# Kernel optimization log

Measured on AMD Instinct MI355X. Metric: run time of the kernel, lower is better.

## Reference

```python
import jax, jax.numpy as jnp
import numpy as np

N = 50000
E = 800000
IN_DIM, HID, OUT = 128, 256, 40
BN_EPS = 1e-5


def setup_inputs() -> dict:
    key = jax.random.key(0)
    ks = jax.random.split(key, 10)
    x = jax.random.normal(ks[0], (N, IN_DIM), dtype=jnp.float32)
    edge_index = jax.random.randint(ks[1], (2, E), 0, N, dtype=jnp.int64)
    W1 = jax.random.normal(ks[2], (IN_DIM, HID), dtype=jnp.float32) * 0.05
    b1 = jnp.zeros((HID,), dtype=jnp.float32)
    W2 = jax.random.normal(ks[3], (HID, HID), dtype=jnp.float32) * 0.05
    b2 = jnp.zeros((HID,), dtype=jnp.float32)
    W3 = jax.random.normal(ks[4], (HID, OUT), dtype=jnp.float32) * 0.05
    b3 = jnp.zeros((OUT,), dtype=jnp.float32)
    # BatchNorm params (shared across the two pre-final layers in the source)
    gamma = jnp.ones((HID,), dtype=jnp.float32)
    beta = jnp.zeros((HID,), dtype=jnp.float32)
    return {"x": x, "edge_index": edge_index, "W1": W1, "b1": b1,
            "W2": W2, "b2": b2, "W3": W3, "b3": b3,
            "gamma": gamma, "beta": beta}


def _gcn_norm(edge_index):
    # add self-loops, compute symmetric normalization D^-1/2 (A+I) D^-1/2
    self_loops = jnp.arange(N, dtype=edge_index.dtype)
    row = jnp.concatenate([edge_index[0], self_loops])
    col = jnp.concatenate([edge_index[1], self_loops])
    deg = jax.ops.segment_sum(jnp.ones_like(row, dtype=jnp.float32), col, num_segments=N)
    dinv = jnp.where(deg > 0, jax.lax.rsqrt(deg), 0.0)
    norm = dinv[row] * dinv[col]  # [E+N]
    return row, col, norm


def _gcn_conv(h, W, b, row, col, norm):
    h = h @ W                              # transform first (smaller msg dim)
    msg = norm[:, None] * h[col]           # [E+N, F] gather
    agg = jax.ops.segment_sum(msg, row, num_segments=N)  # scatter-add
    return agg + b


def _batchnorm(h, gamma, beta):
    mu = jnp.mean(h, axis=0)
    var = jnp.mean((h - mu) ** 2, axis=0)
    return (h - mu) * jax.lax.rsqrt(var + BN_EPS) * gamma + beta


def reference(x, edge_index, W1, b1, W2, b2, W3, b3, gamma, beta):
    row, col, norm = _gcn_norm(edge_index)
    out = _gcn_conv(x, W1, b1, row, col, norm)
    out = jax.nn.relu(_batchnorm(out, gamma, beta))
    out = _gcn_conv(out, W2, b2, row, col, norm)
    out = jax.nn.relu(_batchnorm(out, gamma, beta))  # BN shared in source
    out = _gcn_conv(out, W3, b3, row, col, norm)
    return jax.nn.log_softmax(out, axis=-1)
```

## Files before the change

### kernel.cpp

```cpp
#include <hip/hip_runtime.h>
#include <math.h>

#define NN 50000
#define NE 800000
#define IN_DIM 128
#define HID 256
#define OUT_DIM 40
#define BN_EPS 1e-5f

#define HG 128
#define HW 25000
#define HPASS 12800

#define NBK 196
#define PB 256
#define EPB (NE / PB)

typedef __attribute__((ext_vector_type(8))) short short8;
typedef __attribute__((ext_vector_type(4))) float f32x4;
typedef __attribute__((ext_vector_type(2))) float f32x2;

__device__ __forceinline__ ushort f2bf(float f) {
    union { float f; unsigned u; } v; v.f = f;
    unsigned r = v.u + 0x7fffu + ((v.u >> 16) & 1u);
    return (ushort)(r >> 16);
}
__device__ __forceinline__ unsigned pack2bf(float a, float b) {
    return (unsigned)f2bf(a) | ((unsigned)f2bf(b) << 16);
}
__device__ __forceinline__ float bflo(unsigned u) {
    union { unsigned a; float f; } v; v.a = u << 16; return v.f;
}
__device__ __forceinline__ float bfhi(unsigned u) {
    union { unsigned a; float f; } v; v.a = u & 0xffff0000u; return v.f;
}
__device__ __forceinline__ f32x2 fp8_dec_lo(int v) {
    return __builtin_amdgcn_cvt_pk_f32_fp8(v, false);
}
__device__ __forceinline__ f32x2 fp8_dec_hi(int v) {
    return __builtin_amdgcn_cvt_pk_f32_fp8(v, true);
}
__device__ __forceinline__ int fp8_enc_lo(float a, float b, int old) {
    return __builtin_amdgcn_cvt_pk_fp8_f32(a, b, old, false);
}
__device__ __forceinline__ int fp8_enc_hi(float a, float b, int old) {
    return __builtin_amdgcn_cvt_pk_fp8_f32(a, b, old, true);
}

__global__ __launch_bounds__(512) void k_p1(const int* __restrict__ erow,
                                            const int* __restrict__ ecol,
                                            unsigned* __restrict__ Pcol,
                                            unsigned* __restrict__ cnt) {
    __shared__ unsigned lds[HPASS];
    int t = threadIdx.x;
    int b = blockIdx.x;
    if (b < HG) {
        unsigned* partial = Pcol + (size_t)b * HW;
        int e0 = b * (NE / HG), e1 = e0 + (NE / HG);
#pragma unroll
        for (int pass = 0; pass < 2; pass++) {
            int wbase = pass ? HPASS : 0;
            int wend = pass ? HW : HPASS;
            int nw = wend - wbase;
            for (int w = t; w < HPASS; w += 512) lds[w] = 0u;
            __syncthreads();
            int vlo = wbase * 2, vhi = wend * 2;
            for (int e = e0 + t; e < e1; e += 512) {
                int v = ecol[e];
                if (v >= vlo && v < vhi)
                    atomicAdd(&lds[(v >> 1) - wbase], (v & 1) ? 0x10000u : 1u);
            }
            __syncthreads();
            for (int w = t; w < nw; w += 512) partial[wbase + w] = lds[w];
            __syncthreads();
        }
    } else {
        int bb = b - HG;
        for (int i = t; i < NBK; i += 512) lds[i] = 0u;
        __syncthreads();
        int e0 = bb * EPB;
        for (int i = t; i < EPB; i += 512) atomicAdd(&lds[((unsigned)erow[e0 + i]) >> 8], 1u);
        __syncthreads();
        for (int i = t; i < NBK; i += 512) cnt[bb * NBK + i] = lds[i];
    }
}

__global__ __launch_bounds__(256) void k_p2(const unsigned* __restrict__ Pcol,
                                            float* __restrict__ dinv,
                                            const unsigned* __restrict__ cnt,
                                            unsigned* __restrict__ off,
                                            unsigned* __restrict__ bstart,
                                            float* __restrict__ bnacc) {
    int t = threadIdx.x;
    if (blockIdx.x < 98) {
        int w = blockIdx.x * 256 + t;
        if (w >= HW) return;
        unsigned sc = 0;
        for (int b = 0; b < HG; b++) sc += Pcol[(size_t)b * HW + w];
        dinv[2 * w] = rsqrtf((float)((sc & 0xffffu) + 1u));
        dinv[2 * w + 1] = rsqrtf((float)((sc >> 16) + 1u));
    } else if (blockIdx.x == 98) {
        __shared__ unsigned s[256];
        unsigned tot = 0;
        if (t < NBK) for (int b = 0; b < PB; b++) tot += cnt[b * NBK + t];
        s[t] = tot;
        __syncthreads();
        for (int o = 1; o < 256; o <<= 1) {
            unsigned x = (t >= o) ? s[t - o] : 0u;
            __syncthreads();
            s[t] += x;
            __syncthreads();
        }
        unsigned base = s[t] - tot;
        if (t < NBK) bstart[t] = base;
        if (t == NBK - 1) bstart[NBK] = base + tot;
        if (t < NBK) {
            unsigned run = base;
            for (int b = 0; b < PB; b++) { off[b * NBK + t] = run; run += cnt[b * NBK + t]; }
        }
    } else {
        bnacc[(blockIdx.x - 99) * 256 + t] = 0.f;
    }
}

__global__ __launch_bounds__(256) void k_p3(const int* __restrict__ erow,
                                            const int* __restrict__ ecol,
                                            const unsigned* __restrict__ off,
                                            int2* __restrict__ ebuf,
                                            const float* __restrict__ x,
                                            const float* __restrict__ dinv,
                                            uchar* __restrict__ xs8,
                                            const float* __restrict__ W1,
                                            const float* __restrict__ W2,
                                            const float* __restrict__ W3,
                                            ushort* __restrict__ Wt1,
                                            ushort* __restrict__ Wt2,
                                            ushort* __restrict__ Wt3) {
    int t = threadIdx.x, b = blockIdx.x;
    if (b < PB) {
        __shared__ unsigned c[NBK];
        for (int i = t; i < NBK; i += 256) c[i] = off[b * NBK + i];
        __syncthreads();
        int e0 = b * EPB;
        for (int i = t; i < EPB; i += 256) {
            int r = erow[e0 + i], cc = ecol[e0 + i];
            unsigned p = atomicAdd(&c[((unsigned)r) >> 8], 1u);
            ebuf[p] = make_int2(r, cc);
        }
    } else if (b < PB + 6250) {
        int i = (b - PB) * 256 + t;
        int row = i >> 5;
        float d = dinv[row];
        float4 v = ((const float4*)x)[i];
        int p = fp8_enc_lo(v.x * d, v.y * d, 0);
        p = fp8_enc_hi(v.z * d, v.w * d, p);
        ((int*)xs8)[i] = p;
    } else {
        int i = (b - PB - 6250) * 256 + t;
        if (i < 128 * 256) { int k = i / 256, n = i % 256; Wt1[n * 128 + k] = f2bf(W1[i]); }
        if (i < 256 * 256) { int k = i / 256, n = i % 256; Wt2[n * 256 + k] = f2bf(W2[i]); }
        if (i < 48 * 256)  { int n = i / 256, k = i % 256;
                             Wt3[i] = (n < OUT_DIM) ? f2bf(W3[k * OUT_DIM + n]) : (ushort)0; }
    }
}

__global__ __launch_bounds__(256) void k_part4(const int2* __restrict__ ebuf,
                                               const unsigned* __restrict__ bstart,
                                               unsigned* __restrict__ rowptr,
                                               int* __restrict__ colidx) {
    __shared__ unsigned rc[256], cur[256], s[256];
    int t = threadIdx.x, b = blockIdx.x;
    unsigned ebase = bstart[b], ecnt = bstart[b + 1] - ebase;
    rc[t] = 0u;
    __syncthreads();
    for (unsigned i = t; i < ecnt; i += 256) atomicAdd(&rc[ebuf[ebase + i].x & 255], 1u);
    __syncthreads();
    unsigned v = rc[t];
    s[t] = v;
    __syncthreads();
    for (int o = 1; o < 256; o <<= 1) {
        unsigned x = (t >= o) ? s[t - o] : 0u;
        __syncthreads();
        s[t] += x;
        __syncthreads();
    }
    unsigned excl = s[t] - v;
    int row = (b << 8) + t;
    if (row < NN) rowptr[row] = ebase + excl;
    cur[t] = ebase + excl;
    if (b == 0 && t == 0) rowptr[NN] = NE;
    __syncthreads();
    for (unsigned i = t; i < ecnt; i += 256) {
        int2 e = ebuf[ebase + i];
        unsigned p = atomicAdd(&cur[e.x & 255], 1u);
        colidx[p] = e.y;
    }
}

__global__ __launch_bounds__(64) void k_agg_x(const uchar* __restrict__ xs8,
                                              const unsigned* __restrict__ rowptr,
                                              const int* __restrict__ colidx,
                                              const float* __restrict__ dinv,
                                              ushort* __restrict__ Xa) {
    int r = blockIdx.x;
    int t = threadIdx.x;
    int lane = t & 31, half = t >> 5;
    const unsigned* Xv = (const unsigned*)xs8;
    float a0 = 0.f, a1 = 0.f, a2 = 0.f, a3 = 0.f;
    if (half == 0) {
        unsigned y = Xv[(size_t)r * 32 + lane];
        f32x2 l = fp8_dec_lo((int)y), h = fp8_dec_hi((int)y);
        a0 = l[0]; a1 = l[1]; a2 = h[0]; a3 = h[1];
    }
    unsigned e0 = rowptr[r], e1 = rowptr[r + 1];
    unsigned e = e0 + half;
    for (; e + 6 < e1; e += 8) {
        int c0 = colidx[e], c1 = colidx[e + 2], c2 = colidx[e + 4], c3 = colidx[e + 6];
        unsigned v0 = Xv[(size_t)c0 * 32 + lane];
        unsigned v1 = Xv[(size_t)c1 * 32 + lane];
        unsigned v2 = Xv[(size_t)c2 * 32 + lane];
        unsigned v3 = Xv[(size_t)c3 * 32 + lane];
        f32x2 l0 = fp8_dec_lo((int)v0), h0 = fp8_dec_hi((int)v0);
        f32x2 l1 = fp8_dec_lo((int)v1), h1 = fp8_dec_hi((int)v1);
        f32x2 l2 = fp8_dec_lo((int)v2), h2 = fp8_dec_hi((int)v2);
        f32x2 l3 = fp8_dec_lo((int)v3), h3 = fp8_dec_hi((int)v3);
        a0 += l0[0] + l1[0] + l2[0] + l3[0];
        a1 += l0[1] + l1[1] + l2[1] + l3[1];
        a2 += h0[0] + h1[0] + h2[0] + h3[0];
        a3 += h0[1] + h1[1] + h2[1] + h3[1];
    }
    for (; e < e1; e += 2) {
        unsigned v = Xv[(size_t)colidx[e] * 32 + lane];
        f32x2 l = fp8_dec_lo((int)v), h = fp8_dec_hi((int)v);
        a0 += l[0]; a1 += l[1]; a2 += h[0]; a3 += h[1];
    }
    a0 += __shfl_xor(a0, 32, 64);
    a1 += __shfl_xor(a1, 32, 64);
    a2 += __shfl_xor(a2, 32, 64);
    a3 += __shfl_xor(a3, 32, 64);
    if (half == 0) {
        float dr = dinv[r];
        uint2 o;
        o.x = pack2bf(dr * a0, dr * a1);
        o.y = pack2bf(dr * a2, dr * a3);
        ((uint2*)Xa)[(size_t)r * 32 + lane] = o;
    }
}

template <int K>
__global__ __launch_bounds__(256) void k_gemm1(const ushort* __restrict__ A,
                                               const ushort* __restrict__ Bt,
                                               ushort* __restrict__ H16,
                                               float* __restrict__ bnacc) {
    constexpr int BK = 32;
    constexpr int LD = 40;
    __shared__ ushort sA[64 * LD];
    __shared__ ushort sB[128 * LD];
    int t = threadIdx.x;
    int wave = t >> 6, lane = t & 63;
    int quad = lane >> 4, m15 = lane & 15;
    long r0 = (long)blockIdx.x * 64;
    int n0 = blockIdx.y * 128;

    f32x4 acc[8];
#pragma unroll
    for (int i = 0; i < 8; i++) { acc[i][0] = 0.f; acc[i][1] = 0.f; acc[i][2] = 0.f; acc[i][3] = 0.f; }

    for (int k0 = 0; k0 < K; k0 += BK) {
        {
            int row = t >> 2, seg = (t & 3) * 8;
            long gr = r0 + row;
            uint4 v = make_uint4(0, 0, 0, 0);
            if (gr < NN) v = *(const uint4*)(A + gr * K + k0 + seg);
            *(uint4*)(sA + row * LD + seg) = v;
        }
        {
            int n = t >> 1, seg = (t & 1) * 16;
            const uint4* src = (const uint4*)(Bt + (long)(n0 + n) * K + k0 + seg);
            uint4 b0 = src[0], b1 = src[1];
            *(uint4*)(sB + n * LD + seg) = b0;
            *(uint4*)(sB + n * LD + seg + 8) = b1;
        }
        __syncthreads();
        short8 a = *(const short8*)(sA + (wave * 16 + m15) * LD + quad * 8);
#pragma unroll
        for (int ct = 0; ct < 8; ct++) {
            short8 b = *(const short8*)(sB + (ct * 16 + m15) * LD + quad * 8);
            acc[ct] = __builtin_amdgcn_mfma_f32_16x16x32_bf16(a, b, acc[ct], 0, 0, 0);
        }
        __syncthreads();
    }
    long rowbase = r0 + wave * 16 + quad * 4;
#pragma unroll
    for (int ct = 0; ct < 8; ct++) {
        int col = n0 + ct * 16 + m15;
#pragma unroll
        for (int rg = 0; rg < 4; rg++) {
            long gr = rowbase + rg;
            if (gr < NN) H16[gr * 256 + col] = f2bf(acc[ct][rg]);
        }
    }
    float* ldsS = (float*)(void*)sA;
    float* ldsQ = (float*)(void*)sB;
#pragma unroll
    for (int ct = 0; ct < 8; ct++) {
        float s = acc[ct][0] + acc[ct][1] + acc[ct][2] + acc[ct][3];
        float q = acc[ct][0] * acc[ct][0] + acc[ct][1] * acc[ct][1]
                + acc[ct][2] * acc[ct][2] + acc[ct][3] * acc[ct][3];
        s += __shfl_xor(s, 16, 64); q += __shfl_xor(q, 16, 64);
        s += __shfl_xor(s, 32, 64); q += __shfl_xor(q, 32, 64);
        if (quad == 0) {
            ldsS[wave * 128 + ct * 16 + m15] = s;
            ldsQ[wave * 128 + ct * 16 + m15] = q;
        }
    }
    __syncthreads();
    {
        int c = t & 127;
        int slice = blockIdx.x & 7;
        float v = (t < 128)
            ? ldsS[c] + ldsS[128 + c] + ldsS[256 + c] + ldsS[384 + c]
            : ldsQ[c] + ldsQ[128 + c] + ldsQ[256 + c] + ldsQ[384 + c];
        atomicAdd(&bnacc[slice * 512 + ((t < 128) ? 0 : 256) + n0 + c], v);
    }
}

__device__ __forceinline__ void bn_prolog(const float* __restrict__ bnacc,
                                          const float* __restrict__ gamma,
                                          const float* __restrict__ beta,
                                          float* __restrict__ bnsc,
                                          float* __restrict__ bnsh, int t) {
    float s = 0.f, q = 0.f;
#pragma unroll
    for (int sl = 0; sl < 8; sl++) {
        s += bnacc[sl * 512 + t];
        q += bnacc[sl * 512 + 256 + t];
    }
    float mu = s * (1.f / NN);
    float var = q * (1.f / NN) - mu * mu;
    float g = gamma[t] * rsqrtf(var + BN_EPS);
    bnsc[t] = g;
    bnsh[t] = beta[t] - mu * g;
}

__device__ __forceinline__ void bn_stage8(const ushort* __restrict__ Hrow, bool valid,
                                          const float* __restrict__ bnsc,
                                          const float* __restrict__ bnsh, int col0,
                                          ushort* __restrict__ dst) {
    uint4 hv = make_uint4(0, 0, 0, 0);
    if (valid) hv = *(const uint4*)(Hrow + col0);
    float f[8] = { bflo(hv.x), bfhi(hv.x), bflo(hv.y), bfhi(hv.y),
                   bflo(hv.z), bfhi(hv.z), bflo(hv.w), bfhi(hv.w) };
#pragma unroll
    for (int j = 0; j < 8; j++)
        dst[j] = f2bf(fmaxf(f[j] * bnsc[col0 + j] + bnsh[col0 + j], 0.f));
}

__global__ __launch_bounds__(256) void k_gemm2(const ushort* __restrict__ H16,
                                               const float* __restrict__ bnacc,
                                               const float* __restrict__ gamma,
                                               const float* __restrict__ beta,
                                               const ushort* __restrict__ Bt,
                                               const float* __restrict__ dinv,
                                               uchar* __restrict__ Y8) {
    constexpr int K = 256, BK = 32, LD = 40;
    __shared__ ushort sA[64 * LD];
    __shared__ ushort sB[128 * LD];
    __shared__ float bnsc[256], bnsh[256];
    int t = threadIdx.x;
    int wave = t >> 6, lane = t & 63;
    int quad = lane >> 4, m15 = lane & 15;
    long r0 = (long)blockIdx.x * 64;
    int n0 = blockIdx.y * 128;

    bn_prolog(bnacc, gamma, beta, bnsc, bnsh, t);
    __syncthreads();

    f32x4 acc[8];
#pragma unroll
    for (int i = 0; i < 8; i++) { acc[i][0] = 0.f; acc[i][1] = 0.f; acc[i][2] = 0.f; acc[i][3] = 0.f; }

    for (int k0 = 0; k0 < K; k0 += BK) {
        {
            int row = t >> 2, seg = (t & 3) * 8;
            long gr = r0 + row;
            bn_stage8(H16 + gr * 256, gr < NN, bnsc, bnsh, k0 + seg, sA + row * LD + seg);
        }
        {
            int n = t >> 1, seg = (t & 1) * 16;
            const uint4* src = (const uint4*)(Bt + (long)(n0 + n) * K + k0 + seg);
            uint4 b0 = src[0], b1 = src[1];
            *(uint4*)(sB + n * LD + seg) = b0;
            *(uint4*)(sB + n * LD + seg + 8) = b1;
        }
        __syncthreads();
        short8 a = *(const short8*)(sA + (wave * 16 + m15) * LD + quad * 8);
#pragma unroll
        for (int ct = 0; ct < 8; ct++) {
            short8 b = *(const short8*)(sB + (ct * 16 + m15) * LD + quad * 8);
            acc[ct] = __builtin_amdgcn_mfma_f32_16x16x32_bf16(a, b, acc[ct], 0, 0, 0);
        }
        __syncthreads();
    }
    long rowbase = r0 + wave * 16 + quad * 4;
    float dv[4];
#pragma unroll
    for (int rg = 0; rg < 4; rg++) dv[rg] = (rowbase + rg < NN) ? dinv[rowbase + rg] : 0.f;
#pragma unroll
    for (int ct = 0; ct < 8; ct++) {
        int col = n0 + ct * 16 + m15;
#pragma unroll
        for (int rg = 0; rg < 4; rg++) {
            long gr = rowbase + rg;
            if (gr < NN) {
                int p = fp8_enc_lo(dv[rg] * acc[ct][rg], 0.f, 0);
                Y8[gr * 256 + col] = (uchar)(p & 0xff);
            }
        }
    }
}

__global__ __launch_bounds__(256) void k_gemm3(const ushort* __restrict__ H16,
                                               const float* __restrict__ bnacc,
                                               const float* __restrict__ gamma,
                                               const float* __restrict__ beta,
                                               const ushort* __restrict__ Wt3,
                                               const float* __restrict__ dinv,
                                               ushort* __restrict__ Y) {
    constexpr int LD = 264;
    __shared__ ushort sA[64 * LD];
    __shared__ ushort sB[48 * LD];
    __shared__ float bnsc[256], bnsh[256];
    int t = threadIdx.x;
    int wave = t >> 6, lane = t & 63;
    int quad = lane >> 4, m15 = lane & 15;
    long r0 = (long)blockIdx.x * 64;

    bn_prolog(bnacc, gamma, beta, bnsc, bnsh, t);
    __syncthreads();

    for (int idx = t; idx < 48 * 16; idx += 256) {
        int n = idx >> 4, s = (idx & 15) * 16;
        const uint4* src = (const uint4*)(Wt3 + n * 256 + s);
        *(uint4*)(sB + n * LD + s) = src[0];
        *(uint4*)(sB + n * LD + s + 8) = src[1];
    }
    {
        int row = t >> 2;
        long gr = r0 + row;
#pragma unroll
        for (int s8 = 0; s8 < 8; s8++) {
            int seg = s8 * 32 + (t & 3) * 8;
            bn_stage8(H16 + gr * 256, gr < NN, bnsc, bnsh, seg, sA + row * LD + seg);
        }
    }
    __syncthreads();

    f32x4 acc[3];
#pragma unroll
    for (int i = 0; i < 3; i++) { acc[i][0] = 0.f; acc[i][1] = 0.f; acc[i][2] = 0.f; acc[i][3] = 0.f; }
#pragma unroll
    for (int k0 = 0; k0 < 256; k0 += 32) {
        short8 a = *(const short8*)(sA + (wave * 16 + m15) * LD + k0 + quad * 8);
#pragma unroll
        for (int ct = 0; ct < 3; ct++) {
            short8 b = *(const short8*)(sB + (ct * 16 + m15) * LD + k0 + quad * 8);
            acc[ct] = __builtin_amdgcn_mfma_f32_16x16x32_bf16(a, b, acc[ct], 0, 0, 0);
        }
    }
    long rowbase = r0 + wave * 16 + quad * 4;
#pragma unroll
    for (int ct = 0; ct < 3; ct++) {
        int col = ct * 16 + m15;
#pragma unroll
        for (int rg = 0; rg < 4; rg++) {
            long gr = rowbase + rg;
            if (gr < NN) Y[gr * 64 + col] = f2bf(dinv[gr] * acc[ct][rg]);
        }
    }
}

__global__ __launch_bounds__(64) void k_agg_hid(const uchar* __restrict__ Y8,
                                                const unsigned* __restrict__ rowptr,
                                                const int* __restrict__ colidx,
                                                const float* __restrict__ dinv,
                                                ushort* __restrict__ H16) {
    int r = blockIdx.x;
    int t = threadIdx.x;
    int lane = t & 31, half = t >> 5;
    const uint2* Yv = (const uint2*)Y8;
    float a0 = 0.f, a1 = 0.f, a2 = 0.f, a3 = 0.f, a4 = 0.f, a5 = 0.f, a6 = 0.f, a7 = 0.f;
    if (half == 0) {
        uint2 y = Yv[(size_t)r * 32 + lane];
        f32x2 p0 = fp8_dec_lo((int)y.x), p1 = fp8_dec_hi((int)y.x);
        f32x2 p2 = fp8_dec_lo((int)y.y), p3 = fp8_dec_hi((int)y.y);
        a0 = p0[0]; a1 = p0[1]; a2 = p1[0]; a3 = p1[1];
        a4 = p2[0]; a5 = p2[1]; a6 = p3[0]; a7 = p3[1];
    }
    unsigned e0 = rowptr[r], e1 = rowptr[r + 1];
    unsigned e = e0 + half;
    for (; e + 6 < e1; e += 8) {
        int c0 = colidx[e], c1 = colidx[e + 2], c2 = colidx[e + 4], c3 = colidx[e + 6];
        uint2 v0 = Yv[(size_t)c0 * 32 + lane];
        uint2 v1 = Yv[(size_t)c1 * 32 + lane];
        uint2 v2 = Yv[(size_t)c2 * 32 + lane];
        uint2 v3 = Yv[(size_t)c3 * 32 + lane];
        f32x2 l0x = fp8_dec_lo((int)v0.x), h0x = fp8_dec_hi((int)v0.x);
        f32x2 l0y = fp8_dec_lo((int)v0.y), h0y = fp8_dec_hi((int)v0.y);
        f32x2 l1x = fp8_dec_lo((int)v1.x), h1x = fp8_dec_hi((int)v1.x);
        f32x2 l1y = fp8_dec_lo((int)v1.y), h1y = fp8_dec_hi((int)v1.y);
        f32x2 l2x = fp8_dec_lo((int)v2.x), h2x = fp8_dec_hi((int)v2.x);
        f32x2 l2y = fp8_dec_lo((int)v2.y), h2y = fp8_dec_hi((int)v2.y);
        f32x2 l3x = fp8_dec_lo((int)v3.x), h3x = fp8_dec_hi((int)v3.x);
        f32x2 l3y = fp8_dec_lo((int)v3.y), h3y = fp8_dec_hi((int)v3.y);
        a0 += l0x[0] + l1x[0] + l2x[0] + l3x[0];
        a1 += l0x[1] + l1x[1] + l2x[1] + l3x[1];
        a2 += h0x[0] + h1x[0] + h2x[0] + h3x[0];
        a3 += h0x[1] + h1x[1] + h2x[1] + h3x[1];
        a4 += l0y[0] + l1y[0] + l2y[0] + l3y[0];
        a5 += l0y[1] + l1y[1] + l2y[1] + l3y[1];
        a6 += h0y[0] + h1y[0] + h2y[0] + h3y[0];
        a7 += h0y[1] + h1y[1] + h2y[1] + h3y[1];
    }
    for (; e < e1; e += 2) {
        uint2 v = Yv[(size_t)colidx[e] * 32 + lane];
        f32x2 lx = fp8_dec_lo((int)v.x), hx = fp8_dec_hi((int)v.x);
        f32x2 ly = fp8_dec_lo((int)v.y), hy = fp8_dec_hi((int)v.y);
        a0 += lx[0]; a1 += lx[1]; a2 += hx[0]; a3 += hx[1];
        a4 += ly[0]; a5 += ly[1]; a6 += hy[0]; a7 += hy[1];
    }
    a0 += __shfl_xor(a0, 32, 64); a1 += __shfl_xor(a1, 32, 64);
    a2 += __shfl_xor(a2, 32, 64); a3 += __shfl_xor(a3, 32, 64);
    a4 += __shfl_xor(a4, 32, 64); a5 += __shfl_xor(a5, 32, 64);
    a6 += __shfl_xor(a6, 32, 64); a7 += __shfl_xor(a7, 32, 64);
    if (half == 0) {
        float dr = dinv[r];
        uint4 o;
        o.x = pack2bf(dr * a0, dr * a1);
        o.y = pack2bf(dr * a2, dr * a3);
        o.z = pack2bf(dr * a4, dr * a5);
        o.w = pack2bf(dr * a6, dr * a7);
        ((uint4*)H16)[(size_t)r * 32 + lane] = o;
    }
}

__global__ __launch_bounds__(64) void k_agg_lsm(const ushort* __restrict__ Y,
                                                const unsigned* __restrict__ rowptr,
                                                const int* __restrict__ colidx,
                                                const float* __restrict__ dinv,
                                                const float* __restrict__ b3,
                                                float* __restrict__ out) {
    int r = blockIdx.x;
    int t = threadIdx.x;
    int lane = t & 31, half = t >> 5;
    const unsigned* Yv = (const unsigned*)Y;
    float a0 = 0.f, a1 = 0.f;
    if (half == 0) {
        unsigned y = Yv[(size_t)r * 32 + lane];
        a0 = bflo(y); a1 = bfhi(y);
    }
    unsigned e0 = rowptr[r], e1 = rowptr[r + 1];
    unsigned e = e0 + half;
    for (; e + 6 < e1; e += 8) {
        int c0 = colidx[e], c1 = colidx[e + 2], c2 = colidx[e + 4], c3 = colidx[e + 6];
        unsigned v0 = Yv[(size_t)c0 * 32 + lane];
        unsigned v1 = Yv[(size_t)c1 * 32 + lane];
        unsigned v2 = Yv[(size_t)c2 * 32 + lane];
        unsigned v3 = Yv[(size_t)c3 * 32 + lane];
        a0 += bflo(v0) + bflo(v1) + bflo(v2) + bflo(v3);
        a1 += bfhi(v0) + bfhi(v1) + bfhi(v2) + bfhi(v3);
    }
    for (; e < e1; e += 2) {
        unsigned v = Yv[(size_t)colidx[e] * 32 + lane];
        a0 += bflo(v); a1 += bfhi(v);
    }
    a0 += __shfl_xor(a0, 32, 64);
    a1 += __shfl_xor(a1, 32, 64);
    bool act = (half == 0) && (lane < OUT_DIM / 2);
    float o0 = -1e30f, o1 = -1e30f;
    if (act) {
        float dr = dinv[r];
        o0 = dr * a0 + b3[2 * lane];
        o1 = dr * a1 + b3[2 * lane + 1];
    }
    float m = fmaxf(o0, o1);
#pragma unroll
    for (int d = 1; d < 64; d <<= 1) m = fmaxf(m, __shfl_xor(m, d, 64));
    float ex = act ? (expf(o0 - m) + expf(o1 - m)) : 0.f;
#pragma unroll
    for (int d = 1; d < 64; d <<= 1) ex += __shfl_xor(ex, d, 64);
    float ls = logf(ex) + m;
    if (act) {
        out[(size_t)r * OUT_DIM + 2 * lane] = o0 - ls;
        out[(size_t)r * OUT_DIM + 2 * lane + 1] = o1 - ls;
    }
}

__global__ __launch_bounds__(256) void k_bn_stats2(const ushort* __restrict__ H16,
                                                   float* __restrict__ bnacc) {
    __shared__ float ls[512];
    int t = threadIdx.x;
    ls[t] = 0.f; ls[t + 256] = 0.f;
    __syncthreads();
    int colb = (t & 31) * 8;
    float s[8], q[8];
#pragma unroll
    for (int j = 0; j < 8; j++) { s[j] = 0.f; q[j] = 0.f; }
    for (int rb = blockIdx.x * 8 + (t >> 5); rb < NN; rb += gridDim.x * 8) {
        uint4 v = *(const uint4*)(H16 + (size_t)rb * 256 + colb);
        float f[8] = { bflo(v.x), bfhi(v.x), bflo(v.y), bfhi(v.y),
                       bflo(v.z), bfhi(v.z), bflo(v.w), bfhi(v.w) };
#pragma unroll
        for (int j = 0; j < 8; j++) { s[j] += f[j]; q[j] += f[j] * f[j]; }
    }
#pragma unroll
    for (int j = 0; j < 8; j++) {
        atomicAdd(&ls[colb + j], s[j]);
        atomicAdd(&ls[256 + colb + j], q[j]);
    }
    __syncthreads();
    int slice = blockIdx.x & 7;
    atomicAdd(&bnacc[slice * 512 + t], ls[t]);
    atomicAdd(&bnacc[slice * 512 + 256 + t], ls[t + 256]);
}


extern "C" void kernel_launch(void* const* d_in, const int* in_sizes, int n_in,
                              void* d_out, int out_size, void* d_ws, size_t ws_size,
                              hipStream_t stream) {
    const float* x     = (const float*)d_in[0];
    const int*   erow  = (const int*)d_in[1];
    const int*   ecol  = ((const int*)d_in[1]) + NE;
    const float* W1    = (const float*)d_in[2];
    const float* W2    = (const float*)d_in[4];
    const float* W3    = (const float*)d_in[6];
    const float* b3    = (const float*)d_in[7];
    const float* gamma = (const float*)d_in[8];
    const float* beta  = (const float*)d_in[9];
    float* out = (float*)d_out;

    char* ws = (char*)d_ws;
    size_t off = 0;
    auto alloc = [&](size_t bytes) -> void* {
        void* p = ws + off;
        off = (off + bytes + 255) & ~(size_t)255;
        return p;
    };
    float*    dinv     = (float*)alloc(NN * 4);
    unsigned* rowptr   = (unsigned*)alloc((NN + 1) * 4);
    int*      colidx   = (int*)alloc((size_t)NE * 4);
    float*    bnacc    = (float*)alloc(2 * 8 * 512 * 4);
    unsigned* cnt      = (unsigned*)alloc((size_t)PB * NBK * 4);
    unsigned* boff     = (unsigned*)alloc((size_t)PB * NBK * 4);
    unsigned* bstart   = (unsigned*)alloc((NBK + 1) * 4);
    ushort*   Wt1      = (ushort*)alloc(128 * 256 * 2);
    ushort*   Wt2      = (ushort*)alloc(256 * 256 * 2);
    ushort*   Wt3      = (ushort*)alloc(48 * 256 * 2);
    uchar*    xs8      = (uchar*)alloc((size_t)NN * IN_DIM);
    ushort*   Xa       = (ushort*)alloc((size_t)NN * IN_DIM * 2);
    ushort*   H16      = (ushort*)alloc((size_t)NN * HID * 2);
    uchar*    Ys2      = (uchar*)alloc((size_t)NN * HID);
    ushort*   Ys3      = (ushort*)alloc((size_t)NN * 64 * 2);

    float* bnacc1 = bnacc;
    float* bnacc2 = bnacc + 8 * 512;

    unsigned* Pcol = (unsigned*)H16;
    int2*     ebuf = (int2*)((char*)H16 + (size_t)13 * 1024 * 1024);

    k_p1<<<HG + PB, 512, 0, stream>>>(erow, ecol, Pcol, cnt);
    k_p2<<<99 + 32, 256, 0, stream>>>(Pcol, dinv, cnt, boff, bstart, bnacc);
    k_p3<<<PB + 6250 + 256, 256, 0, stream>>>(erow, ecol, boff, ebuf,
                                              x, dinv, xs8, W1, W2, W3, Wt1, Wt2, Wt3);
    k_part4<<<NBK, 256, 0, stream>>>(ebuf, bstart, rowptr, colidx);

    dim3 ggrid((NN + 63) / 64, 2);

    k_agg_x<<<NN, 64, 0, stream>>>(xs8, rowptr, colidx, dinv, Xa);
    k_gemm1<IN_DIM><<<ggrid, 256, 0, stream>>>(Xa, Wt1, H16, bnacc1);

    k_gemm2<<<ggrid, 256, 0, stream>>>(H16, bnacc1, gamma, beta, Wt2, dinv, Ys2);
    k_agg_hid<<<NN, 64, 0, stream>>>(Ys2, rowptr, colidx, dinv, H16);
    k_bn_stats2<<<1024, 256, 0, stream>>>(H16, bnacc2);

    k_gemm3<<<(NN + 63) / 64, 256, 0, stream>>>(H16, bnacc2, gamma, beta, Wt3, dinv, Ys3);
    k_agg_lsm<<<NN, 64, 0, stream>>>(Ys3, rowptr, colidx, dinv, b3, out);
}
```

Baseline: 313.5 us.

## Double GEMM row tile to 128 so each wave reuses B fragments

The first two GEMM kernels now give each block 128 rows instead of 64, and each wave computes two 16-row MFMA tiles that share the same B fragment loaded from LDS. This halves the number of B-tile loads and LDS B reads per output row and halves the grid size. In exchange, accumulator register use doubles, which may lower occupancy, and with fewer blocks there is less parallelism to hide latency. The BN stats reduction and the epilogues are adjusted to cover both row tiles.

```diff
diff --git a/kernel.cpp b/kernel.cpp
--- a/kernel.cpp
+++ b/kernel.cpp
@@ -254,25 +254,31 @@
                                                float* __restrict__ bnacc) {
     constexpr int BK = 32;
     constexpr int LD = 40;
-    __shared__ ushort sA[64 * LD];
+    __shared__ ushort sA[128 * LD];
     __shared__ ushort sB[128 * LD];
     int t = threadIdx.x;
     int wave = t >> 6, lane = t & 63;
     int quad = lane >> 4, m15 = lane & 15;
-    long r0 = (long)blockIdx.x * 64;
+    long r0 = (long)blockIdx.x * 128;
     int n0 = blockIdx.y * 128;
 
-    f32x4 acc[8];
-#pragma unroll
-    for (int i = 0; i < 8; i++) { acc[i][0] = 0.f; acc[i][1] = 0.f; acc[i][2] = 0.f; acc[i][3] = 0.f; }
+    f32x4 acc[2][8];
+#pragma unroll
+    for (int rt = 0; rt < 2; rt++)
+#pragma unroll
+        for (int i = 0; i < 8; i++) { acc[rt][i][0] = 0.f; acc[rt][i][1] = 0.f; acc[rt][i][2] = 0.f; acc[rt][i][3] = 0.f; }
 
     for (int k0 = 0; k0 < K; k0 += BK) {
         {
-            int row = t >> 2, seg = (t & 3) * 8;
+            int row = t >> 1, seg = (t & 1) * 16;
             long gr = r0 + row;
-            uint4 v = make_uint4(0, 0, 0, 0);
-            if (gr < NN) v = *(const uint4*)(A + gr * K + k0 + seg);
-            *(uint4*)(sA + row * LD + seg) = v;
+            uint4 v0 = make_uint4(0, 0, 0, 0), v1 = v0;
+            if (gr < NN) {
+                const uint4* src = (const uint4*)(A + gr * K + k0 + seg);
+                v0 = src[0]; v1 = src[1];
+            }
+            *(uint4*)(sA + row * LD + seg) = v0;
+            *(uint4*)(sA + row * LD + seg + 8) = v1;
         }
         {
             int n = t >> 1, seg = (t & 1) * 16;
@@ -282,31 +288,40 @@
             *(uint4*)(sB + n * LD + seg + 8) = b1;
         }
         __syncthreads();
-        short8 a = *(const short8*)(sA + (wave * 16 + m15) * LD + quad * 8);
+        short8 a0 = *(const short8*)(sA + (wave * 32 + m15) * LD + quad * 8);
+        short8 a1 = *(const short8*)(sA + (wave * 32 + 16 + m15) * LD + quad * 8);
 #pragma unroll
         for (int ct = 0; ct < 8; ct++) {
             short8 b = *(const short8*)(sB + (ct * 16 + m15) * LD + quad * 8);
-            acc[ct] = __builtin_amdgcn_mfma_f32_16x16x32_bf16(a, b, acc[ct], 0, 0, 0);
-        }
-        __syncthreads();
-    }
-    long rowbase = r0 + wave * 16 + quad * 4;
-#pragma unroll
-    for (int ct = 0; ct < 8; ct++) {
-        int col = n0 + ct * 16 + m15;
-#pragma unroll
-        for (int rg = 0; rg < 4; rg++) {
-            long gr = rowbase + rg;
-            if (gr < NN) H16[gr * 256 + col] = f2bf(acc[ct][rg]);
+            acc[0][ct] = __builtin_amdgcn_mfma_f32_16x16x32_bf16(a0, b, acc[0][ct], 0, 0, 0);
+            acc[1][ct] = __builtin_amdgcn_mfma_f32_16x16x32_bf16(a1, b, acc[1][ct], 0, 0, 0);
+        }
+        __syncthreads();
+    }
+#pragma unroll
+    for (int rt = 0; rt < 2; rt++) {
+        long rowbase = r0 + wave * 32 + rt * 16 + quad * 4;
+#pragma unroll
+        for (int ct = 0; ct < 8; ct++) {
+            int col = n0 + ct * 16 + m15;
+#pragma unroll
+            for (int rg = 0; rg < 4; rg++) {
+                long gr = rowbase + rg;
+                if (gr < NN) H16[gr * 256 + col] = f2bf(acc[rt][ct][rg]);
+            }
         }
     }
     float* ldsS = (float*)(void*)sA;
     float* ldsQ = (float*)(void*)sB;
 #pragma unroll
     for (int ct = 0; ct < 8; ct++) {
-        float s = acc[ct][0] + acc[ct][1] + acc[ct][2] + acc[ct][3];
-        float q = acc[ct][0] * acc[ct][0] + acc[ct][1] * acc[ct][1]
-                + acc[ct][2] * acc[ct][2] + acc[ct][3] * acc[ct][3];
+        float s = 0.f, q = 0.f;
+#pragma unroll
+        for (int rt = 0; rt < 2; rt++) {
+            s += acc[rt][ct][0] + acc[rt][ct][1] + acc[rt][ct][2] + acc[rt][ct][3];
+            q += acc[rt][ct][0] * acc[rt][ct][0] + acc[rt][ct][1] * acc[rt][ct][1]
+               + acc[rt][ct][2] * acc[rt][ct][2] + acc[rt][ct][3] * acc[rt][ct][3];
+        }
         s += __shfl_xor(s, 16, 64); q += __shfl_xor(q, 16, 64);
         s += __shfl_xor(s, 32, 64); q += __shfl_xor(q, 32, 64);
         if (quad == 0) {
@@ -364,27 +379,30 @@
                                                const float* __restrict__ dinv,
                                                uchar* __restrict__ Y8) {
     constexpr int K = 256, BK = 32, LD = 40;
-    __shared__ ushort sA[64 * LD];
+    __shared__ ushort sA[128 * LD];
     __shared__ ushort sB[128 * LD];
     __shared__ float bnsc[256], bnsh[256];
     int t = threadIdx.x;
     int wave = t >> 6, lane = t & 63;
     int quad = lane >> 4, m15 = lane & 15;
-    long r0 = (long)blockIdx.x * 64;
+    long r0 = (long)blockIdx.x * 128;
     int n0 = blockIdx.y * 128;
 
     bn_prolog(bnacc, gamma, beta, bnsc, bnsh, t);
     __syncthreads();
 
-    f32x4 acc[8];
-#pragma unroll
-    for (int i = 0; i < 8; i++) { acc[i][0] = 0.f; acc[i][1] = 0.f; acc[i][2] = 0.f; acc[i][3] = 0.f; }
+    f32x4 acc[2][8];
+#pragma unroll
+    for (int rt = 0; rt < 2; rt++)
+#pragma unroll
+        for (int i = 0; i < 8; i++) { acc[rt][i][0] = 0.f; acc[rt][i][1] = 0.f; acc[rt][i][2] = 0.f; acc[rt][i][3] = 0.f; }
 
     for (int k0 = 0; k0 < K; k0 += BK) {
         {
-            int row = t >> 2, seg = (t & 3) * 8;
+            int row = t >> 1, seg = (t & 1) * 16;
             long gr = r0 + row;
             bn_stage8(H16 + gr * 256, gr < NN, bnsc, bnsh, k0 + seg, sA + row * LD + seg);
+            bn_stage8(H16 + gr * 256, gr < NN, bnsc, bnsh, k0 + seg + 8, sA + row * LD + seg + 8);
         }
         {
             int n = t >> 1, seg = (t & 1) * 16;
@@ -394,27 +412,32 @@
             *(uint4*)(sB + n * LD + seg + 8) = b1;
         }
         __syncthreads();
-        short8 a = *(const short8*)(sA + (wave * 16 + m15) * LD + quad * 8);
+        short8 a0 = *(const short8*)(sA + (wave * 32 + m15) * LD + quad * 8);
+        short8 a1 = *(const short8*)(sA + (wave * 32 + 16 + m15) * LD + quad * 8);
 #pragma unroll
         for (int ct = 0; ct < 8; ct++) {
             short8 b = *(const short8*)(sB + (ct * 16 + m15) * LD + quad * 8);
-            acc[ct] = __builtin_amdgcn_mfma_f32_16x16x32_bf16(a, b, acc[ct], 0, 0, 0);
-        }
-        __syncthreads();
-    }
-    long rowbase = r0 + wave * 16 + quad * 4;
-    float dv[4];
-#pragma unroll
-    for (int rg = 0; rg < 4; rg++) dv[rg] = (rowbase + rg < NN) ? dinv[rowbase + rg] : 0.f;
-#pragma unroll
-    for (int ct = 0; ct < 8; ct++) {
-        int col = n0 + ct * 16 + m15;
-#pragma unroll
-        for (int rg = 0; rg < 4; rg++) {
-            long gr = rowbase + rg;
-            if (gr < NN) {
-                int p = fp8_enc_lo(dv[rg] * acc[ct][rg], 0.f, 0);
-                Y8[gr * 256 + col] = (uchar)(p & 0xff);
+            acc[0][ct] = __builtin_amdgcn_mfma_f32_16x16x32_bf16(a0, b, acc[0][ct], 0, 0, 0);
+            acc[1][ct] = __builtin_amdgcn_mfma_f32_16x16x32_bf16(a1, b, acc[1][ct], 0, 0, 0);
+        }
+        __syncthreads();
+    }
+#pragma unroll
+    for (int rt = 0; rt < 2; rt++) {
+        long rowbase = r0 + wave * 32 + rt * 16 + quad * 4;
+        float dv[4];
+#pragma unroll
+        for (int rg = 0; rg < 4; rg++) dv[rg] = (rowbase + rg < NN) ? dinv[rowbase + rg] : 0.f;
+#pragma unroll
+        for (int ct = 0; ct < 8; ct++) {
+            int col = n0 + ct * 16 + m15;
+#pragma unroll
+            for (int rg = 0; rg < 4; rg++) {
+                long gr = rowbase + rg;
+                if (gr < NN) {
+                    int p = fp8_enc_lo(dv[rg] * acc[rt][ct][rg], 0.f, 0);
+                    Y8[gr * 256 + col] = (uchar)(p & 0xff);
+                }
             }
         }
     }
@@ -674,7 +697,7 @@
                                               x, dinv, xs8, W1, W2, W3, Wt1, Wt2, Wt3);
     k_part4<<<NBK, 256, 0, stream>>>(ebuf, bstart, rowptr, colidx);
 
-    dim3 ggrid((NN + 63) / 64, 2);
+    dim3 ggrid((NN + 127) / 128, 2);
 
     k_agg_x<<<NN, 64, 0, stream>>>(xs8, rowptr, colidx, dinv, Xa);
     k_gemm1<IN_DIM><<<ggrid, 256, 0, stream>>>(Xa, Wt1, H16, bnacc1);
```

Result: slower. 324.6 us (+3.5%).
